# Kernel optimization log

Hardware: AMD Instinct MI355X
Metric: run time of the kernel (lower is better)

## Reference

```python
import jax, jax.numpy as jnp
import numpy as np

B, S, E = 2, 2048, 1024
H, D = 16, 64  # num_heads, head_size; H*D == E

def setup_inputs() -> dict:
    key = jax.random.key(0)
    k1, k2, k3 = jax.random.split(key, 3)
    x = jax.random.normal(k1, (B, S, E), dtype=jnp.float32)
    w_qkv = jax.random.normal(k2, (E, 3 * H * D), dtype=jnp.float32) / np.sqrt(E)
    b_qkv = jnp.zeros((3 * H * D,), dtype=jnp.float32)
    w_out = jax.random.normal(k3, (H * D, E), dtype=jnp.float32) / np.sqrt(H * D)
    b_out = jnp.zeros((E,), dtype=jnp.float32)
    return {"x": x, "w_qkv": w_qkv, "b_qkv": b_qkv, "w_out": w_out, "b_out": b_out}

def reference(x, w_qkv, b_qkv, w_out, b_out):
    b, s, e = x.shape
    qkv = x @ w_qkv + b_qkv                       # [b, s, 3*H*D]
    qkv = qkv.reshape(b, s, 3, H, D).transpose(2, 0, 3, 1, 4)  # [3, b, H, s, D]
    q, k, v = qkv[0], qkv[1], qkv[2]
    scores = jnp.einsum('bhqd,bhkd->bhqk', q, k) / jnp.sqrt(jnp.float32(D))
    mask = jnp.tril(jnp.ones((s, s), dtype=scores.dtype))
    scores = scores * mask - 1e10 * (1 - mask)
    attn = jax.nn.softmax(scores, axis=-1)
    out = jnp.einsum('bhqk,bhkd->bhqd', attn, v)  # [b, H, s, D]
    out = out.transpose(0, 2, 1, 3).reshape(b, s, H * D)
    return out @ w_out + b_out
```

## Files before the change

### kernel.cpp

```cpp
#include <hip/hip_runtime.h>

typedef unsigned short u16;
typedef __attribute__((ext_vector_type(8))) short bf16x8;
typedef __attribute__((ext_vector_type(4))) float f32x4;

#define S_LEN 2048
#define MTOT  4096
#define LOG2E_DIV8 0.1803368784f

__device__ inline u16 f2bf(float f) {
  union { float f; unsigned u; } x; x.f = f;
  unsigned r = x.u + 0x7fffu + ((x.u >> 16) & 1u);
  return (u16)(r >> 16);
}
__device__ inline float bf2f(u16 u) {
  union { unsigned u; float f; } x; x.u = ((unsigned)u) << 16;
  return x.f;
}

__device__ __forceinline__ unsigned cvtpk_bf16(float lo, float hi) {
  unsigned r;
  asm("v_cvt_pk_bf16_f32 %0, %1, %2" : "=v"(r) : "v"(lo), "v"(hi));
  return r;
}
__device__ __forceinline__ float fexp2(float x) {
  float r;
  asm("v_exp_f32 %0, %1" : "=v"(r) : "v"(x));
  return r;
}
__device__ __forceinline__ float frcp(float x) {
  float r;
  asm("v_rcp_f32 %0, %1" : "=v"(r) : "v"(x));
  return r;
}

#define SWAP32(a, b) asm("v_permlane32_swap_b32 %0, %1" : "+v"(a), "+v"(b))
#define SWAP16(a, b) asm("v_permlane16_swap_b32 %0, %1" : "+v"(a), "+v"(b))

__device__ __forceinline__ float sum_lg(float x) {
  float a = x, b = x;
  SWAP32(a, b);
  float s = a + b;
  float c = s, d = s;
  SWAP16(c, d);
  return c + d;
}

typedef __attribute__((address_space(1))) const unsigned int gu32;
typedef __attribute__((address_space(3))) unsigned int lu32;
__device__ __forceinline__ void gload_lds16(const void* g, void* l) {
  __builtin_amdgcn_global_load_lds((gu32*)g, (lu32*)l, 16, 0, 0);
}

#define MFMA16(a, b, c) __builtin_amdgcn_mfma_f32_16x16x32_bf16((a), (b), (c), 0, 0, 0)

__global__ __launch_bounds__(256) void cast_bf16(const float* __restrict__ src,
                                                 u16* __restrict__ dst, int n) {
  int i = (blockIdx.x * 256 + threadIdx.x) * 4;
  if (i >= n) return;
  float4 v = *(const float4*)(src + i);
  ushort4 o;
  o.x = f2bf(v.x); o.y = f2bf(v.y); o.z = f2bf(v.z); o.w = f2bf(v.w);
  *(ushort4*)(dst + i) = o;
}

__global__ __launch_bounds__(256) void transcast_w(const float* __restrict__ wqkv,
                                                   const float* __restrict__ wout,
                                                   u16* __restrict__ dqkv,
                                                   u16* __restrict__ dwout) {
  __shared__ float tile[64][65];
  const float* src; u16* dst; int N, n0;
  if (blockIdx.x < 48) { src = wqkv; dst = dqkv; N = 3072; n0 = blockIdx.x * 64; }
  else                 { src = wout; dst = dwout; N = 1024; n0 = (blockIdx.x - 48) * 64; }
  int K = 1024, k0 = blockIdx.y * 64;
  int t = threadIdx.x;
  for (int i = 0; i < 16; ++i) {
    int idx = t + 256 * i;
    int r = idx >> 6, c = idx & 63;
    tile[r][c] = src[(size_t)(k0 + r) * N + n0 + c];
  }
  __syncthreads();
  for (int i = 0; i < 16; ++i) {
    int idx = t + 256 * i;
    int r = idx >> 6, c = idx & 63;
    dst[(size_t)(n0 + r) * K + k0 + c] = f2bf(tile[c][r]);
  }
}

template<int OUT_BF16>
__global__ __launch_bounds__(256) void gemm_bt(const u16* __restrict__ A,
                                               const u16* __restrict__ Bt,
                                               const float* __restrict__ bias,
                                               void* __restrict__ Cv,
                                               int N, int K,
                                               int qcols, float qscale) {
  __shared__ __align__(16) u16 As[128 * 32];
  __shared__ __align__(16) u16 Bs[128 * 32];
  int t = threadIdx.x;
  int w = t >> 6, l = t & 63;
  int wr = w >> 1, wc = w & 1;
  int lr = l & 15, lg = l >> 4;

  int nwg = gridDim.x * gridDim.y;
  int bid = blockIdx.y * gridDim.x + blockIdx.x;
  int orig = (bid & 7) * (nwg >> 3) + (bid >> 3);
  int bx = orig % gridDim.x, by = orig / gridDim.x;
  int m0 = by * 128, n0 = bx * 128;

  f32x4 acc[4][4];
#pragma unroll
  for (int i = 0; i < 4; ++i)
#pragma unroll
    for (int j = 0; j < 4; ++j)
      acc[i][j] = f32x4{0.f, 0.f, 0.f, 0.f};

  int r0 = w * 32 + (l >> 2);
  int r1 = r0 + 16;
  int c0 = (l & 3) ^ ((r0 >> 1) & 3);
  int c1 = (l & 3) ^ ((r1 >> 1) & 3);
  const u16* gA0 = A + (size_t)(m0 + r0) * K + c0 * 8;
  const u16* gA1 = A + (size_t)(m0 + r1) * K + c1 * 8;
  const u16* gB0 = Bt + (size_t)(n0 + r0) * K + c0 * 8;
  const u16* gB1 = Bt + (size_t)(n0 + r1) * K + c1 * 8;
  u16* lA0 = As + (w * 32) * 32;
  u16* lA1 = As + (w * 32 + 16) * 32;
  u16* lB0 = Bs + (w * 32) * 32;
  u16* lB1 = Bs + (w * 32 + 16) * 32;

  for (int k0 = 0; k0 < K; k0 += 32) {
    gload_lds16(gA0 + k0, lA0);
    gload_lds16(gA1 + k0, lA1);
    gload_lds16(gB0 + k0, lB0);
    gload_lds16(gB1 + k0, lB1);
    __syncthreads();
    bf16x8 af[4], bfr[4];
#pragma unroll
    for (int mi = 0; mi < 4; ++mi) {
      int row = wr * 64 + mi * 16 + lr;
      af[mi] = *(const bf16x8*)(As + row * 32 + ((lg ^ ((row >> 1) & 3)) << 3));
    }
#pragma unroll
    for (int ni = 0; ni < 4; ++ni) {
      int row = wc * 64 + ni * 16 + lr;
      bfr[ni] = *(const bf16x8*)(Bs + row * 32 + ((lg ^ ((row >> 1) & 3)) << 3));
    }
    __builtin_amdgcn_s_setprio(1);
#pragma unroll
    for (int mi = 0; mi < 4; ++mi)
#pragma unroll
      for (int ni = 0; ni < 4; ++ni)
        acc[mi][ni] = MFMA16(af[mi], bfr[ni], acc[mi][ni]);
    __builtin_amdgcn_s_setprio(0);
    __syncthreads();
  }

#pragma unroll
  for (int mi = 0; mi < 4; ++mi)
#pragma unroll
    for (int ni = 0; ni < 4; ++ni)
#pragma unroll
      for (int rg = 0; rg < 4; ++rg) {
        int row = m0 + wr * 64 + mi * 16 + lg * 4 + rg;
        int col = n0 + wc * 64 + ni * 16 + lr;
        float v = acc[mi][ni][rg] + bias[col];
        if (col < qcols) v *= qscale;
        if (OUT_BF16) ((u16*)Cv)[(size_t)row * N + col] = f2bf(v);
        else          ((float*)Cv)[(size_t)row * N + col] = v;
      }
}

__global__ __launch_bounds__(256) void gemm_bt64(const u16* __restrict__ A,
                                                 const u16* __restrict__ Bt,
                                                 const float* __restrict__ bias,
                                                 float* __restrict__ C,
                                                 int N, int K) {
  __shared__ __align__(16) u16 As[64 * 32];
  __shared__ __align__(16) u16 Bs[128 * 32];
  int t = threadIdx.x;
  int w = t >> 6, l = t & 63;
  int lr = l & 15, lg = l >> 4;

  int nwg = gridDim.x * gridDim.y;
  int bid = blockIdx.y * gridDim.x + blockIdx.x;
  int orig = (bid & 7) * (nwg >> 3) + (bid >> 3);
  int bx = orig % gridDim.x, by = orig / gridDim.x;
  int m0 = by * 64, n0 = bx * 128;

  f32x4 acc[4][2];
#pragma unroll
  for (int i = 0; i < 4; ++i)
#pragma unroll
    for (int j = 0; j < 2; ++j)
      acc[i][j] = f32x4{0.f, 0.f, 0.f, 0.f};

  int ra = w * 16 + (l >> 2);
  int ca = (l & 3) ^ ((ra >> 1) & 3);
  int rb1 = ra + 64;
  int cb1 = (l & 3) ^ ((rb1 >> 1) & 3);
  const u16* gA  = A  + (size_t)(m0 + ra) * K + ca * 8;
  const u16* gB0 = Bt + (size_t)(n0 + ra) * K + ca * 8;
  const u16* gB1 = Bt + (size_t)(n0 + rb1) * K + cb1 * 8;
  u16* lA  = As + (w * 16) * 32;
  u16* lB0 = Bs + (w * 16) * 32;
  u16* lB1 = Bs + (64 + w * 16) * 32;

  for (int k0 = 0; k0 < K; k0 += 32) {
    gload_lds16(gA + k0, lA);
    gload_lds16(gB0 + k0, lB0);
    gload_lds16(gB1 + k0, lB1);
    __syncthreads();
    bf16x8 af[4], bfr[2];
#pragma unroll
    for (int mi = 0; mi < 4; ++mi) {
      int row = mi * 16 + lr;
      af[mi] = *(const bf16x8*)(As + row * 32 + ((lg ^ ((row >> 1) & 3)) << 3));
    }
#pragma unroll
    for (int ni = 0; ni < 2; ++ni) {
      int row = w * 32 + ni * 16 + lr;
      bfr[ni] = *(const bf16x8*)(Bs + row * 32 + ((lg ^ ((row >> 1) & 3)) << 3));
    }
    __builtin_amdgcn_s_setprio(1);
#pragma unroll
    for (int mi = 0; mi < 4; ++mi)
#pragma unroll
      for (int ni = 0; ni < 2; ++ni)
        acc[mi][ni] = MFMA16(af[mi], bfr[ni], acc[mi][ni]);
    __builtin_amdgcn_s_setprio(0);
    __syncthreads();
  }

#pragma unroll
  for (int mi = 0; mi < 4; ++mi)
#pragma unroll
    for (int ni = 0; ni < 2; ++ni)
#pragma unroll
      for (int rg = 0; rg < 4; ++rg) {
        int row = m0 + mi * 16 + lg * 4 + rg;
        int col = n0 + w * 32 + ni * 16 + lr;
        C[(size_t)row * N + col] = acc[mi][ni][rg] + bias[col];
      }
}

__global__ __launch_bounds__(256) void vtrans(const u16* __restrict__ qkv,
                                              u16* __restrict__ Vt) {
  __shared__ __align__(16) u16 tile[64][72];
  int s0 = blockIdx.x * 64;
  int bh = blockIdx.y;
  int b = bh >> 4, h = bh & 15;
  int t = threadIdx.x;
  for (int c = 0; c < 2; ++c) {
    int idx = t + 256 * c;
    int r = idx >> 3, off = (idx & 7) * 8;
    *(uint4*)(&tile[r][off]) =
        *(const uint4*)(qkv + (size_t)(b * S_LEN + s0 + r) * 3072 + 2048 + h * 64 + off);
  }
  __syncthreads();
  int d = t >> 2, sb = (t & 3) * 16;
  __align__(16) u16 tmp[16];
  for (int j = 0; j < 16; ++j) tmp[j] = tile[sb + j][d];
  u16* dst = Vt + (size_t)(bh * 64 + d) * S_LEN + s0 + sb;
  *(uint4*)(dst) = *(uint4*)(tmp);
  *(uint4*)(dst + 8) = *(uint4*)(tmp + 8);
}

__device__ __forceinline__ void attn_tile(const u16* Ks, const u16* Vs,
                                          bf16x8 q0, bf16x8 q1, f32x4* o,
                                          float& l_run, bool diag,
                                          int w, int l, int lr, int lg) {
  f32x4 s[4];
  __builtin_amdgcn_s_setprio(1);
#pragma unroll
  for (int ct = 0; ct < 4; ++ct) {
    int row = ct * 16 + lr;
    bf16x8 kf0 = *(const bf16x8*)(Ks + ((row * 64 + lg * 8) ^ ((row & 7) << 3)));
    bf16x8 kf1 = *(const bf16x8*)(Ks + ((row * 64 + 32 + lg * 8) ^ ((row & 7) << 3)));
    f32x4 z = f32x4{0.f, 0.f, 0.f, 0.f};
    z = MFMA16(kf0, q0, z);
    z = MFMA16(kf1, q1, z);
    s[ct] = z;
  }
  __builtin_amdgcn_s_setprio(0);
  if (diag) {
    int qrel = w * 16 + lr;
#pragma unroll
    for (int ct = 0; ct < 4; ++ct)
#pragma unroll
      for (int rg = 0; rg < 4; ++rg)
        if ((ct * 16 + lg * 4 + rg) > qrel) s[ct][rg] = -1e30f;
  }
  float ps = 0.f;
#pragma unroll
  for (int ct = 0; ct < 4; ++ct)
#pragma unroll
    for (int rg = 0; rg < 4; ++rg) {
      float p = fexp2(s[ct][rg]);
      s[ct][rg] = p;
      ps += p;
    }
  l_run += sum_lg(ps);

  unsigned W00 = cvtpk_bf16(s[0][0], s[0][1]);
  unsigned W01 = cvtpk_bf16(s[0][2], s[0][3]);
  unsigned W10 = cvtpk_bf16(s[1][0], s[1][1]);
  unsigned W11 = cvtpk_bf16(s[1][2], s[1][3]);
  unsigned W20 = cvtpk_bf16(s[2][0], s[2][1]);
  unsigned W21 = cvtpk_bf16(s[2][2], s[2][3]);
  unsigned W30 = cvtpk_bf16(s[3][0], s[3][1]);
  unsigned W31 = cvtpk_bf16(s[3][2], s[3][3]);
  SWAP32(W00, W10); SWAP16(W00, W10);
  SWAP32(W01, W11); SWAP16(W01, W11);
  SWAP32(W20, W30); SWAP16(W20, W30);
  SWAP32(W21, W31); SWAP16(W21, W31);
  union { unsigned u[4]; bf16x8 v; } P0, P1;
  P0.u[0] = W00; P0.u[1] = W01; P0.u[2] = W10; P0.u[3] = W11;
  P1.u[0] = W20; P1.u[1] = W21; P1.u[2] = W30; P1.u[3] = W31;

  __builtin_amdgcn_s_setprio(1);
#pragma unroll
  for (int dt = 0; dt < 4; ++dt) {
    int row = dt * 16 + lr;
    bf16x8 vf0 = *(const bf16x8*)(Vs + ((row * 64 + lg * 8) ^ ((row & 7) << 3)));
    bf16x8 vf1 = *(const bf16x8*)(Vs + ((row * 64 + 32 + lg * 8) ^ ((row & 7) << 3)));
    o[dt] = MFMA16(P0.v, vf0, o[dt]);
    o[dt] = MFMA16(P1.v, vf1, o[dt]);
  }
  __builtin_amdgcn_s_setprio(0);
}

__global__ __launch_bounds__(256, 4) void attn_kernel(const u16* __restrict__ qkv,
                                                      const u16* __restrict__ Vt,
                                                      u16* __restrict__ po0,
                                                      u16* __restrict__ po1,
                                                      float* __restrict__ pl) {
  __shared__ __align__(16) u16 Ks[2][64 * 64];
  __shared__ __align__(16) u16 Vs[2][64 * 64];
  int bid = blockIdx.y * 32 + blockIdx.x;
  int orig = (bid & 7) * 128 + (bid >> 3);
  int half = orig & 1;
  int qtA = (orig >> 1) & 15;
  int bh = orig >> 5;
  int qtB = 31 - qtA;
  int m = (qtA >= 8) ? 8 : (15 - qtA);
  int kts = half ? m : 0;
  int kte = half ? (qtB + 1) : m;
  int b = bh >> 4, h = bh & 15;
  int t = threadIdx.x, w = t >> 6, l = t & 63;
  int lr = l & 15, lg = l >> 4;

  const u16* qbase = qkv + (size_t)b * S_LEN * 3072 + h * 64;
  int qrA = qtA * 64 + w * 16 + lr;
  int qrB = qtB * 64 + w * 16 + lr;
  bf16x8 qA0 = *(const bf16x8*)(qbase + (size_t)qrA * 3072 + lg * 8);
  bf16x8 qA1 = *(const bf16x8*)(qbase + (size_t)qrA * 3072 + 32 + lg * 8);
  bf16x8 qB0 = *(const bf16x8*)(qbase + (size_t)qrB * 3072 + lg * 8);
  bf16x8 qB1 = *(const bf16x8*)(qbase + (size_t)qrB * 3072 + 32 + lg * 8);

  f32x4 oA[4], oB[4];
#pragma unroll
  for (int i = 0; i < 4; ++i) { oA[i] = f32x4{0.f,0.f,0.f,0.f}; oB[i] = f32x4{0.f,0.f,0.f,0.f}; }
  float lA = 0.f, lB = 0.f;

  int r0s = t >> 3, r1s = r0s + 32;
  int soff = (t & 7) * 8;
  int e0 = (r0s * 64 + soff) ^ ((r0s & 7) << 3);
  int e1 = (r1s * 64 + soff) ^ ((r1s & 7) << 3);
  const u16* Kg = qkv + (size_t)b * S_LEN * 3072 + 1024 + h * 64 + soff;
  const u16* Vg = Vt + (size_t)bh * 64 * S_LEN + soff;

  uint4 k0r, k1r, v0r, v1r;
#define ISSUE(KT) {                                                     \
    int kk0 = (KT) * 64;                                                \
    k0r = *(const uint4*)(Kg + (size_t)(kk0 + r0s) * 3072);             \
    k1r = *(const uint4*)(Kg + (size_t)(kk0 + r1s) * 3072);             \
    v0r = *(const uint4*)(Vg + (size_t)r0s * S_LEN + kk0);              \
    v1r = *(const uint4*)(Vg + (size_t)r1s * S_LEN + kk0);              }

  ISSUE(kts);
  *(uint4*)(Ks[0] + e0) = k0r;
  *(uint4*)(Ks[0] + e1) = k1r;
  *(uint4*)(Vs[0] + e0) = v0r;
  *(uint4*)(Vs[0] + e1) = v1r;
  if (kts + 1 < kte) ISSUE(kts + 1);
  __syncthreads();

  int cur = 0;
  for (int kt = kts; kt < kte; ++kt) {
    if (kt + 1 < kte) {
      u16* Kd = Ks[cur ^ 1];
      u16* Vd = Vs[cur ^ 1];
      *(uint4*)(Kd + e0) = k0r;
      *(uint4*)(Kd + e1) = k1r;
      *(uint4*)(Vd + e0) = v0r;
      *(uint4*)(Vd + e1) = v1r;
    }
    if (kt + 2 < kte) ISSUE(kt + 2);
    const u16* Kc = Ks[cur];
    const u16* Vc = Vs[cur];
    if (kt <= qtA)
      attn_tile(Kc, Vc, qA0, qA1, oA, lA, kt == qtA, w, l, lr, lg);
    attn_tile(Kc, Vc, qB0, qB1, oB, lB, kt == qtB, w, l, lr, lg);
    __syncthreads();
    cur ^= 1;
  }
#undef ISSUE

  u16* po = half ? po1 : po0;
  float* plh = pl + half * 65536;
#pragma unroll
  for (int dt = 0; dt < 4; ++dt)
#pragma unroll
    for (int rg = 0; rg < 4; ++rg) {
      int d = dt * 16 + lr;
      int qA_ = qtA * 64 + w * 16 + lg * 4 + rg;
      int qB_ = qtB * 64 + w * 16 + lg * 4 + rg;
      po[(size_t)(b * S_LEN + qA_) * 1024 + h * 64 + d] = f2bf(oA[dt][rg]);
      po[(size_t)(b * S_LEN + qB_) * 1024 + h * 64 + d] = f2bf(oB[dt][rg]);
    }
  if (lg == 0) {
    plh[bh * 2048 + qtA * 64 + w * 16 + lr] = lA;
    plh[bh * 2048 + qtB * 64 + w * 16 + lr] = lB;
  }
}

__global__ __launch_bounds__(256) void attn_combine(const u16* po0,
                                                    const u16* __restrict__ po1,
                                                    const float* __restrict__ pl,
                                                    u16* out) {
  int i = (blockIdx.x * 256 + threadIdx.x) * 8;
  int row = i >> 10;
  int h = (i & 1023) >> 6;
  int bh = (row >> 11) * 16 + h;
  int q = row & 2047;
  float r = frcp(pl[bh * 2048 + q] + pl[65536 + bh * 2048 + q]);
  bf16x8 a = *(const bf16x8*)(po0 + i);
  bf16x8 c = *(const bf16x8*)(po1 + i);
  union { u16 u[8]; bf16x8 v; } o;
#pragma unroll
  for (int j = 0; j < 8; ++j)
    o.u[j] = f2bf((bf2f((u16)a[j]) + bf2f((u16)c[j])) * r);
  *(bf16x8*)(out + i) = o.v;
}

extern "C" void kernel_launch(void* const* d_in, const int* in_sizes, int n_in,
                              void* d_out, int out_size, void* d_ws, size_t ws_size,
                              hipStream_t stream) {
  const float* x     = (const float*)d_in[0];
  const float* w_qkv = (const float*)d_in[1];
  const float* b_qkv = (const float*)d_in[2];
  const float* w_out = (const float*)d_in[3];
  const float* b_out = (const float*)d_in[4];
  float* out = (float*)d_out;

  char* ws = (char*)d_ws;
  u16* x_bf   = (u16*)(ws);
  u16* po1    = (u16*)(ws);
  u16* wqkvT  = (u16*)(ws + ( 8ull << 20));
  float* pl   = (float*)(ws + ( 8ull << 20));
  u16* woutT  = (u16*)(ws + (14ull << 20));
  u16* qkv    = (u16*)(ws + (16ull << 20));
  u16* Vt     = (u16*)(ws + (40ull << 20));
  u16* po0    = (u16*)(ws + (48ull << 20));
  u16* attnb  = (u16*)(ws + (48ull << 20));

  cast_bf16<<<MTOT * 1024 / 1024, 256, 0, stream>>>(x, x_bf, MTOT * 1024);
  transcast_w<<<dim3(64, 16), 256, 0, stream>>>(w_qkv, w_out, wqkvT, woutT);
  gemm_bt<1><<<dim3(24, 32), 256, 0, stream>>>(x_bf, wqkvT, b_qkv, (void*)qkv,
                                               3072, 1024, 1024, LOG2E_DIV8);
  vtrans<<<dim3(32, 32), 256, 0, stream>>>(qkv, Vt);
  attn_kernel<<<dim3(32, 32), 256, 0, stream>>>(qkv, Vt, po0, po1, pl);
  attn_combine<<<MTOT * 1024 / (256 * 8), 256, 0, stream>>>(po0, po1, pl, attnb);
  gemm_bt64<<<dim3(8, 64), 256, 0, stream>>>(attnb, woutT, b_out, out, 1024, 1024);
}
```

Measured before the change: 113.2 us.

## Fuse attention split-combine into output GEMM and merge prep kernels

Removes the separate attn_combine kernel by having the output projection GEMM load both partial attention outputs and their normalisers, combine and rescale them in registers, and write the bf16 result into LDS as the A tile. The x cast and weight transpose-cast kernels are also merged into one launch. This saves a full read-write round trip of the combined attention tensor and two kernel launches. In exchange, each GEMM block reloads the partials for every N tile (eight times redundantly), and the A path changes from async global-to-LDS loads to register loads with prefetch.

```diff
diff --git a/kernel.cpp b/kernel.cpp
--- a/kernel.cpp
+++ b/kernel.cpp
@@ -54,35 +54,38 @@
 
 #define MFMA16(a, b, c) __builtin_amdgcn_mfma_f32_16x16x32_bf16((a), (b), (c), 0, 0, 0)
 
-__global__ __launch_bounds__(256) void cast_bf16(const float* __restrict__ src,
-                                                 u16* __restrict__ dst, int n) {
-  int i = (blockIdx.x * 256 + threadIdx.x) * 4;
-  if (i >= n) return;
-  float4 v = *(const float4*)(src + i);
-  ushort4 o;
-  o.x = f2bf(v.x); o.y = f2bf(v.y); o.z = f2bf(v.z); o.w = f2bf(v.w);
-  *(ushort4*)(dst + i) = o;
-}
-
-__global__ __launch_bounds__(256) void transcast_w(const float* __restrict__ wqkv,
-                                                   const float* __restrict__ wout,
-                                                   u16* __restrict__ dqkv,
-                                                   u16* __restrict__ dwout) {
+__global__ __launch_bounds__(256) void prep(const float* __restrict__ x,
+                                            const float* __restrict__ wqkv,
+                                            const float* __restrict__ wout,
+                                            u16* __restrict__ x_bf,
+                                            u16* __restrict__ dqkv,
+                                            u16* __restrict__ dwout) {
   __shared__ float tile[64][65];
+  int bid = blockIdx.x;
+  int t = threadIdx.x;
+  if (bid < 4096) {
+    int i = (bid * 256 + t) * 4;
+    float4 v = *(const float4*)(x + i);
+    ushort4 o;
+    o.x = f2bf(v.x); o.y = f2bf(v.y); o.z = f2bf(v.z); o.w = f2bf(v.w);
+    *(ushort4*)(x_bf + i) = o;
+    return;
+  }
+  int idx = bid - 4096;
+  int bx = idx & 63, by = idx >> 6;
   const float* src; u16* dst; int N, n0;
-  if (blockIdx.x < 48) { src = wqkv; dst = dqkv; N = 3072; n0 = blockIdx.x * 64; }
-  else                 { src = wout; dst = dwout; N = 1024; n0 = (blockIdx.x - 48) * 64; }
-  int K = 1024, k0 = blockIdx.y * 64;
-  int t = threadIdx.x;
+  if (bx < 48) { src = wqkv; dst = dqkv; N = 3072; n0 = bx * 64; }
+  else         { src = wout; dst = dwout; N = 1024; n0 = (bx - 48) * 64; }
+  int K = 1024, k0 = by * 64;
   for (int i = 0; i < 16; ++i) {
-    int idx = t + 256 * i;
-    int r = idx >> 6, c = idx & 63;
+    int id2 = t + 256 * i;
+    int r = id2 >> 6, c = id2 & 63;
     tile[r][c] = src[(size_t)(k0 + r) * N + n0 + c];
   }
   __syncthreads();
   for (int i = 0; i < 16; ++i) {
-    int idx = t + 256 * i;
-    int r = idx >> 6, c = idx & 63;
+    int id2 = t + 256 * i;
+    int r = id2 >> 6, c = id2 & 63;
     dst[(size_t)(n0 + r) * K + k0 + c] = f2bf(tile[c][r]);
   }
 }
@@ -169,11 +172,13 @@
       }
 }
 
-__global__ __launch_bounds__(256) void gemm_bt64(const u16* __restrict__ A,
-                                                 const u16* __restrict__ Bt,
-                                                 const float* __restrict__ bias,
-                                                 float* __restrict__ C,
-                                                 int N, int K) {
+__global__ __launch_bounds__(256) void gemm2_fused(const u16* __restrict__ po0,
+                                                   const u16* __restrict__ po1,
+                                                   const float* __restrict__ pl,
+                                                   const u16* __restrict__ Bt,
+                                                   const float* __restrict__ bias,
+                                                   float* __restrict__ C) {
+  const int N = 1024, K = 1024;
   __shared__ __align__(16) u16 As[64 * 32];
   __shared__ __align__(16) u16 Bs[128 * 32];
   int t = threadIdx.x;
@@ -193,21 +198,47 @@
     for (int j = 0; j < 2; ++j)
       acc[i][j] = f32x4{0.f, 0.f, 0.f, 0.f};
 
-  int ra = w * 16 + (l >> 2);
-  int ca = (l & 3) ^ ((ra >> 1) & 3);
-  int rb1 = ra + 64;
+  int ra = w * 16 + (l >> 2), ca = l & 3;
+  int rowg = m0 + ra;
+  const u16* gA0 = po0 + (size_t)rowg * K + ca * 8;
+  const u16* gA1 = po1 + (size_t)rowg * K + ca * 8;
+  const float* plb = pl + (rowg >> 11) * 32768 + (rowg & 2047);
+  u16* lA = As + ra * 32 + ((ca ^ ((ra >> 1) & 3)) << 3);
+
+  int rb = w * 16 + (l >> 2);
+  int cb0 = (l & 3) ^ ((rb >> 1) & 3);
+  int rb1 = rb + 64;
   int cb1 = (l & 3) ^ ((rb1 >> 1) & 3);
-  const u16* gA  = A  + (size_t)(m0 + ra) * K + ca * 8;
-  const u16* gB0 = Bt + (size_t)(n0 + ra) * K + ca * 8;
+  const u16* gB0 = Bt + (size_t)(n0 + rb) * K + cb0 * 8;
   const u16* gB1 = Bt + (size_t)(n0 + rb1) * K + cb1 * 8;
-  u16* lA  = As + (w * 16) * 32;
   u16* lB0 = Bs + (w * 16) * 32;
   u16* lB1 = Bs + (64 + w * 16) * 32;
 
+  uint4 a0r, a1r;
+  float rl0, rl1;
+#define ISSA(K0) {                                                       \
+    a0r = *(const uint4*)(gA0 + (K0));                                   \
+    a1r = *(const uint4*)(gA1 + (K0));                                   \
+    int hh = ((K0) + ca * 8) >> 6;                                       \
+    rl0 = plb[hh * 2048];                                                \
+    rl1 = plb[65536 + hh * 2048];                                        }
+
+  ISSA(0);
   for (int k0 = 0; k0 < K; k0 += 32) {
-    gload_lds16(gA + k0, lA);
     gload_lds16(gB0 + k0, lB0);
     gload_lds16(gB1 + k0, lB1);
+    float rr = frcp(rl0 + rl1);
+    union { uint4 q; unsigned u[4]; } A0, A1, O;
+    A0.q = a0r; A1.q = a1r;
+#pragma unroll
+    for (int j = 0; j < 4; ++j) {
+      union { unsigned u; float f; } lo0, hi0, lo1, hi1;
+      lo0.u = A0.u[j] << 16;  hi0.u = A0.u[j] & 0xffff0000u;
+      lo1.u = A1.u[j] << 16;  hi1.u = A1.u[j] & 0xffff0000u;
+      O.u[j] = cvtpk_bf16((lo0.f + lo1.f) * rr, (hi0.f + hi1.f) * rr);
+    }
+    *(uint4*)lA = O.q;
+    if (k0 + 32 < K) ISSA(k0 + 32);
     __syncthreads();
     bf16x8 af[4], bfr[2];
 #pragma unroll
@@ -229,6 +260,7 @@
     __builtin_amdgcn_s_setprio(0);
     __syncthreads();
   }
+#undef ISSA
 
 #pragma unroll
   for (int mi = 0; mi < 4; ++mi)
@@ -423,25 +455,6 @@
   }
 }
 
-__global__ __launch_bounds__(256) void attn_combine(const u16* po0,
-                                                    const u16* __restrict__ po1,
-                                                    const float* __restrict__ pl,
-                                                    u16* out) {
-  int i = (blockIdx.x * 256 + threadIdx.x) * 8;
-  int row = i >> 10;
-  int h = (i & 1023) >> 6;
-  int bh = (row >> 11) * 16 + h;
-  int q = row & 2047;
-  float r = frcp(pl[bh * 2048 + q] + pl[65536 + bh * 2048 + q]);
-  bf16x8 a = *(const bf16x8*)(po0 + i);
-  bf16x8 c = *(const bf16x8*)(po1 + i);
-  union { u16 u[8]; bf16x8 v; } o;
-#pragma unroll
-  for (int j = 0; j < 8; ++j)
-    o.u[j] = f2bf((bf2f((u16)a[j]) + bf2f((u16)c[j])) * r);
-  *(bf16x8*)(out + i) = o.v;
-}
-
 extern "C" void kernel_launch(void* const* d_in, const int* in_sizes, int n_in,
                               void* d_out, int out_size, void* d_ws, size_t ws_size,
                               hipStream_t stream) {
@@ -461,14 +474,11 @@
   u16* qkv    = (u16*)(ws + (16ull << 20));
   u16* Vt     = (u16*)(ws + (40ull << 20));
   u16* po0    = (u16*)(ws + (48ull << 20));
-  u16* attnb  = (u16*)(ws + (48ull << 20));
-
-  cast_bf16<<<MTOT * 1024 / 1024, 256, 0, stream>>>(x, x_bf, MTOT * 1024);
-  transcast_w<<<dim3(64, 16), 256, 0, stream>>>(w_qkv, w_out, wqkvT, woutT);
+
+  prep<<<4096 + 1024, 256, 0, stream>>>(x, w_qkv, w_out, x_bf, wqkvT, woutT);
   gemm_bt<1><<<dim3(24, 32), 256, 0, stream>>>(x_bf, wqkvT, b_qkv, (void*)qkv,
                                                3072, 1024, 1024, LOG2E_DIV8);
   vtrans<<<dim3(32, 32), 256, 0, stream>>>(qkv, Vt);
   attn_kernel<<<dim3(32, 32), 256, 0, stream>>>(qkv, Vt, po0, po1, pl);
-  attn_combine<<<MTOT * 1024 / (256 * 8), 256, 0, stream>>>(po0, po1, pl, attnb);
-  gemm_bt64<<<dim3(8, 64), 256, 0, stream>>>(attnb, woutT, b_out, out, 1024, 1024);
-}
+  gemm2_fused<<<dim3(8, 64), 256, 0, stream>>>(po0, po1, pl, woutT, b_out, out);
+}
```

Measured after the change: 115.5 us. +2.1%, slower.

## Merge cast kernels and fuse V transpose into QKV GEMM epilogue

Applied to the files above, without the earlier changes.

Combines the x cast and the weight transpose-cast into a single prep launch, and removes the separate vtrans kernel. The QKV GEMM now writes the V columns directly in transposed layout, staging them through shared memory. This saves two kernel launches and a full read/write pass over V. The cost is a more complex epilogue with extra barriers in the V blocks, and the V portion of the qkv buffer is no longer written.

```diff
diff --git a/kernel.cpp b/kernel.cpp
--- a/kernel.cpp
+++ b/kernel.cpp
@@ -54,48 +54,53 @@
 
 #define MFMA16(a, b, c) __builtin_amdgcn_mfma_f32_16x16x32_bf16((a), (b), (c), 0, 0, 0)
 
-__global__ __launch_bounds__(256) void cast_bf16(const float* __restrict__ src,
-                                                 u16* __restrict__ dst, int n) {
-  int i = (blockIdx.x * 256 + threadIdx.x) * 4;
-  if (i >= n) return;
-  float4 v = *(const float4*)(src + i);
-  ushort4 o;
-  o.x = f2bf(v.x); o.y = f2bf(v.y); o.z = f2bf(v.z); o.w = f2bf(v.w);
-  *(ushort4*)(dst + i) = o;
-}
-
-__global__ __launch_bounds__(256) void transcast_w(const float* __restrict__ wqkv,
-                                                   const float* __restrict__ wout,
-                                                   u16* __restrict__ dqkv,
-                                                   u16* __restrict__ dwout) {
+__global__ __launch_bounds__(256) void prep(const float* __restrict__ x,
+                                            const float* __restrict__ wqkv,
+                                            const float* __restrict__ wout,
+                                            u16* __restrict__ x_bf,
+                                            u16* __restrict__ dqkv,
+                                            u16* __restrict__ dwout) {
   __shared__ float tile[64][65];
+  int bid = blockIdx.x;
+  int t = threadIdx.x;
+  if (bid < 4096) {
+    int i = (bid * 256 + t) * 4;
+    float4 v = *(const float4*)(x + i);
+    ushort4 o;
+    o.x = f2bf(v.x); o.y = f2bf(v.y); o.z = f2bf(v.z); o.w = f2bf(v.w);
+    *(ushort4*)(x_bf + i) = o;
+    return;
+  }
+  int idx = bid - 4096;
+  int bx = idx & 63, by = idx >> 6;
   const float* src; u16* dst; int N, n0;
-  if (blockIdx.x < 48) { src = wqkv; dst = dqkv; N = 3072; n0 = blockIdx.x * 64; }
-  else                 { src = wout; dst = dwout; N = 1024; n0 = (blockIdx.x - 48) * 64; }
-  int K = 1024, k0 = blockIdx.y * 64;
-  int t = threadIdx.x;
+  if (bx < 48) { src = wqkv; dst = dqkv; N = 3072; n0 = bx * 64; }
+  else         { src = wout; dst = dwout; N = 1024; n0 = (bx - 48) * 64; }
+  int K = 1024, k0 = by * 64;
   for (int i = 0; i < 16; ++i) {
-    int idx = t + 256 * i;
-    int r = idx >> 6, c = idx & 63;
+    int id2 = t + 256 * i;
+    int r = id2 >> 6, c = id2 & 63;
     tile[r][c] = src[(size_t)(k0 + r) * N + n0 + c];
   }
   __syncthreads();
   for (int i = 0; i < 16; ++i) {
-    int idx = t + 256 * i;
-    int r = idx >> 6, c = idx & 63;
+    int id2 = t + 256 * i;
+    int r = id2 >> 6, c = id2 & 63;
     dst[(size_t)(n0 + r) * K + k0 + c] = f2bf(tile[c][r]);
   }
 }
 
-template<int OUT_BF16>
-__global__ __launch_bounds__(256) void gemm_bt(const u16* __restrict__ A,
-                                               const u16* __restrict__ Bt,
-                                               const float* __restrict__ bias,
-                                               void* __restrict__ Cv,
-                                               int N, int K,
-                                               int qcols, float qscale) {
-  __shared__ __align__(16) u16 As[128 * 32];
-  __shared__ __align__(16) u16 Bs[128 * 32];
+__global__ __launch_bounds__(256) void gemm_qkv(const u16* __restrict__ A,
+                                                const u16* __restrict__ Bt,
+                                                const float* __restrict__ bias,
+                                                u16* __restrict__ qkv,
+                                                u16* __restrict__ Vt,
+                                                float qscale) {
+  const int N = 3072, K = 1024;
+  __shared__ __align__(16) u16 smem[8704];
+  u16* As = smem;
+  u16* Bs = smem + 4096;
+  u16* Vl = smem;
   int t = threadIdx.x;
   int w = t >> 6, l = t & 63;
   int wr = w >> 1, wc = w & 1;
@@ -154,19 +159,51 @@
     __syncthreads();
   }
 
-#pragma unroll
-  for (int mi = 0; mi < 4; ++mi)
-#pragma unroll
-    for (int ni = 0; ni < 4; ++ni)
-#pragma unroll
-      for (int rg = 0; rg < 4; ++rg) {
-        int row = m0 + wr * 64 + mi * 16 + lg * 4 + rg;
-        int col = n0 + wc * 64 + ni * 16 + lr;
-        float v = acc[mi][ni][rg] + bias[col];
-        if (col < qcols) v *= qscale;
-        if (OUT_BF16) ((u16*)Cv)[(size_t)row * N + col] = f2bf(v);
-        else          ((float*)Cv)[(size_t)row * N + col] = v;
-      }
+  if (n0 < 2048) {
+#pragma unroll
+    for (int mi = 0; mi < 4; ++mi)
+#pragma unroll
+      for (int ni = 0; ni < 4; ++ni)
+#pragma unroll
+        for (int rg = 0; rg < 4; ++rg) {
+          int row = m0 + wr * 64 + mi * 16 + lg * 4 + rg;
+          int col = n0 + wc * 64 + ni * 16 + lr;
+          float v = acc[mi][ni][rg] + bias[col];
+          if (col < 1024) v *= qscale;
+          qkv[(size_t)row * N + col] = f2bf(v);
+        }
+    return;
+  }
+
+  int b = m0 >> 11, sbase = m0 & 2047;
+#pragma unroll
+  for (int p = 0; p < 2; ++p) {
+    __syncthreads();
+    if (wc == p) {
+#pragma unroll
+      for (int mi = 0; mi < 4; ++mi)
+#pragma unroll
+        for (int ni = 0; ni < 4; ++ni) {
+          int cl = ni * 16 + lr;
+          int rl = wr * 64 + mi * 16 + lg * 4;
+          int col = n0 + p * 64 + cl;
+          union { u16 u[4]; unsigned long long q; } pk;
+#pragma unroll
+          for (int rg = 0; rg < 4; ++rg)
+            pk.u[rg] = f2bf(acc[mi][ni][rg] + bias[col]);
+          *(unsigned long long*)&Vl[cl * 136 + rl] = pk.q;
+        }
+    }
+    __syncthreads();
+    int hv = ((n0 - 2048) >> 6) + p;
+    int c = t >> 2;
+    int r0w = (t & 3) * 32;
+    u16* dst = Vt + ((size_t)((b * 16 + hv) * 64 + c)) * S_LEN + sbase + r0w;
+    const u16* srcl = Vl + c * 136 + r0w;
+#pragma unroll
+    for (int j = 0; j < 4; ++j)
+      *(uint4*)(dst + j * 8) = *(const uint4*)(srcl + j * 8);
+  }
 }
 
 __global__ __launch_bounds__(256) void gemm_bt64(const u16* __restrict__ A,
@@ -240,28 +277,6 @@
         int col = n0 + w * 32 + ni * 16 + lr;
         C[(size_t)row * N + col] = acc[mi][ni][rg] + bias[col];
       }
-}
-
-__global__ __launch_bounds__(256) void vtrans(const u16* __restrict__ qkv,
-                                              u16* __restrict__ Vt) {
-  __shared__ __align__(16) u16 tile[64][72];
-  int s0 = blockIdx.x * 64;
-  int bh = blockIdx.y;
-  int b = bh >> 4, h = bh & 15;
-  int t = threadIdx.x;
-  for (int c = 0; c < 2; ++c) {
-    int idx = t + 256 * c;
-    int r = idx >> 3, off = (idx & 7) * 8;
-    *(uint4*)(&tile[r][off]) =
-        *(const uint4*)(qkv + (size_t)(b * S_LEN + s0 + r) * 3072 + 2048 + h * 64 + off);
-  }
-  __syncthreads();
-  int d = t >> 2, sb = (t & 3) * 16;
-  __align__(16) u16 tmp[16];
-  for (int j = 0; j < 16; ++j) tmp[j] = tile[sb + j][d];
-  u16* dst = Vt + (size_t)(bh * 64 + d) * S_LEN + s0 + sb;
-  *(uint4*)(dst) = *(uint4*)(tmp);
-  *(uint4*)(dst + 8) = *(uint4*)(tmp + 8);
 }
 
 __device__ __forceinline__ void attn_tile(const u16* Ks, const u16* Vs,
@@ -463,11 +478,9 @@
   u16* po0    = (u16*)(ws + (48ull << 20));
   u16* attnb  = (u16*)(ws + (48ull << 20));
 
-  cast_bf16<<<MTOT * 1024 / 1024, 256, 0, stream>>>(x, x_bf, MTOT * 1024);
-  transcast_w<<<dim3(64, 16), 256, 0, stream>>>(w_qkv, w_out, wqkvT, woutT);
-  gemm_bt<1><<<dim3(24, 32), 256, 0, stream>>>(x_bf, wqkvT, b_qkv, (void*)qkv,
-                                               3072, 1024, 1024, LOG2E_DIV8);
-  vtrans<<<dim3(32, 32), 256, 0, stream>>>(qkv, Vt);
+  prep<<<4096 + 1024, 256, 0, stream>>>(x, w_qkv, w_out, x_bf, wqkvT, woutT);
+  gemm_qkv<<<dim3(24, 32), 256, 0, stream>>>(x_bf, wqkvT, b_qkv, qkv, Vt,
+                                             LOG2E_DIV8);
   attn_kernel<<<dim3(32, 32), 256, 0, stream>>>(qkv, Vt, po0, po1, pl);
   attn_combine<<<MTOT * 1024 / (256 * 8), 256, 0, stream>>>(po0, po1, pl, attnb);
   gemm_bt64<<<dim3(8, 64), 256, 0, stream>>>(attnb, woutT, b_out, out, 1024, 1024);
```

After: 120.2 us. 1.06x slower.
